# Kernel optimization log

Hardware: AMD Instinct MI355X
Metric: run time of the kernel (lower is better)

The kernel has to match this reference:

```python
import jax, jax.numpy as jnp
import numpy as np

N_USERS = 100000
EMBED_DIM = 128
N_EDGES = 640000


def setup_inputs() -> dict:
    key = jax.random.key(0)
    k1, k2, k3, k4, k5, k6 = jax.random.split(key, 6)
    # Xavier-normal-ish scale for embedding table
    emb = jax.random.normal(k1, (N_USERS, EMBED_DIM), dtype=jnp.float32) * 0.02
    s = 1.0 / np.sqrt(EMBED_DIM)
    W_l = jax.random.normal(k2, (EMBED_DIM, EMBED_DIM), dtype=jnp.float32) * s
    b_l = jax.random.normal(k3, (EMBED_DIM,), dtype=jnp.float32) * 0.01
    W_r = jax.random.normal(k4, (EMBED_DIM, EMBED_DIM), dtype=jnp.float32) * s
    src = jax.random.randint(k5, (N_EDGES,), 0, N_USERS, dtype=jnp.int64)
    dst = jax.random.randint(k6, (N_EDGES,), 0, N_USERS, dtype=jnp.int64)
    return {"emb": emb, "W_l": W_l, "b_l": b_l, "W_r": W_r, "src": src, "dst": dst}


def reference(emb, W_l, b_l, W_r, src, dst):
    # GraphSAGE (mean aggr) over the full user embedding table.
    # messages gathered from source nodes: [E, D]
    msgs = emb[src]
    agg = jax.ops.segment_sum(msgs, dst, num_segments=N_USERS)  # [N, D]
    deg = jax.ops.segment_sum(jnp.ones((dst.shape[0],), dtype=emb.dtype), dst,
                              num_segments=N_USERS)
    agg = agg / jnp.maximum(deg, 1.0)[:, None]  # mean over neighbors
    # out = lin_l(mean neighbors) + lin_r(self); bias on lin_l only (PyG SAGEConv)
    out = agg @ W_l.T + b_l + emb @ W_r.T
    # dropout (p=0) and batchnorm (is_norm=False) are identity here
    return out
```

## Files before the change

kernel.cpp:

```cpp
#include <hip/hip_runtime.h>
#include <hip/hip_bf16.h>

#define N_USERS   100000
#define EMBED_DIM 128
#define N_EDGES   640000
#define ZERO_ROW  N_USERS

typedef __bf16 bf16x8 __attribute__((ext_vector_type(8)));
typedef float  f32x4  __attribute__((ext_vector_type(4)));

#define OFF_COUNTS 25600256
#define OFF_TOTAL  26000256
#define OFF_START  26000384
#define OFF_CURSOR 26400384
#define OFF_PERM   26800384
#define OFF_WLSW   30560384
#define OFF_WRSW   30593152
#define OFF_AGGB   30625920

__device__ __forceinline__ unsigned short f2bf_rne(float f) {
    union { float f; unsigned u; } c; c.f = f;
    unsigned u = c.u + 0x7fffu + ((c.u >> 16) & 1u);
    return (unsigned short)(u >> 16);
}
__device__ __forceinline__ float bf2f_lo(unsigned u) {
    union { float f; unsigned u; } c; c.u = u << 16;
    return c.f;
}
__device__ __forceinline__ float bf2f_hi(unsigned u) {
    union { float f; unsigned u; } c; c.u = u & 0xffff0000u;
    return c.f;
}

__global__ __launch_bounds__(256) void k_init(const float* __restrict__ emb,
                                              const float* __restrict__ Wl,
                                              const float* __restrict__ Wr,
                                              const int* __restrict__ dst,
                                              unsigned short* __restrict__ embb,
                                              int* __restrict__ counts,
                                              unsigned short* __restrict__ wlsw,
                                              unsigned short* __restrict__ wrsw) {
    int i = blockIdx.x * 256 + threadIdx.x;
    if (i < 2048) {
        int li = i & 63;
        int kt = (i >> 6) & 3;
        int jt = i >> 8;
        int row  = jt * 16 + (li & 15);
        int colb = kt * 32 + ((li >> 4) << 3);
        const float4* pl = (const float4*)(Wl + row * 128 + colb);
        const float4* pr = (const float4*)(Wr + row * 128 + colb);
        float4 l0 = pl[0], l1 = pl[1];
        float4 r0 = pr[0], r1 = pr[1];
        int o = i * 8;
        wlsw[o+0] = f2bf_rne(l0.x); wlsw[o+1] = f2bf_rne(l0.y);
        wlsw[o+2] = f2bf_rne(l0.z); wlsw[o+3] = f2bf_rne(l0.w);
        wlsw[o+4] = f2bf_rne(l1.x); wlsw[o+5] = f2bf_rne(l1.y);
        wlsw[o+6] = f2bf_rne(l1.z); wlsw[o+7] = f2bf_rne(l1.w);
        wrsw[o+0] = f2bf_rne(r0.x); wrsw[o+1] = f2bf_rne(r0.y);
        wrsw[o+2] = f2bf_rne(r0.z); wrsw[o+3] = f2bf_rne(r0.w);
        wrsw[o+4] = f2bf_rne(r1.x); wrsw[o+5] = f2bf_rne(r1.y);
        wrsw[o+6] = f2bf_rne(r1.z); wrsw[o+7] = f2bf_rne(r1.w);
    }
    if (i < 16) {
        int4 z = {0, 0, 0, 0};
        ((int4*)(embb + (size_t)ZERO_ROW * EMBED_DIM))[i] = z;
    }
    float4 a = ((const float4*)emb)[i * 2 + 0];
    float4 b = ((const float4*)emb)[i * 2 + 1];
    int4 p;
    p.x = (int)f2bf_rne(a.x) | ((int)f2bf_rne(a.y) << 16);
    p.y = (int)f2bf_rne(a.z) | ((int)f2bf_rne(a.w) << 16);
    p.z = (int)f2bf_rne(b.x) | ((int)f2bf_rne(b.y) << 16);
    p.w = (int)f2bf_rne(b.z) | ((int)f2bf_rne(b.w) << 16);
    ((int4*)embb)[i] = p;
    if (i < N_EDGES) atomicAdd(&counts[dst[i]], 1);
}

__global__ __launch_bounds__(256) void k_alloc(const int* __restrict__ counts,
                                               int* __restrict__ start,
                                               int* __restrict__ cursor,
                                               int* __restrict__ total,
                                               int* __restrict__ perm) {
    int i    = blockIdx.x * 256 + threadIdx.x;
    int lane = threadIdx.x & 63;
    int wv   = threadIdx.x >> 6;
    int4 c4 = {0, 0, 0, 0};
    if (i < 25000) c4 = ((const int4*)counts)[i];
    int4 p4;
    p4.x = (c4.x + 3) & ~3;
    p4.y = (c4.y + 3) & ~3;
    p4.z = (c4.z + 3) & ~3;
    p4.w = (c4.w + 3) & ~3;
    int csum = p4.x + p4.y + p4.z + p4.w;
    int pre = csum;
#pragma unroll
    for (int d = 1; d < 64; d <<= 1) {
        int v = __shfl_up(pre, d);
        if (lane >= d) pre += v;
    }
    __shared__ int swv[4];
    __shared__ int sgbase;
    if (lane == 63) swv[wv] = pre;
    __syncthreads();
    if (threadIdx.x == 0)
        sgbase = atomicAdd(total, swv[0] + swv[1] + swv[2] + swv[3]);
    __syncthreads();
    int waveoff = 0;
    for (int w = 0; w < wv; w++) waveoff += swv[w];
    int base = sgbase + waveoff + (pre - csum);
    if (i < 25000) {
        int4 s;
        s.x = base;
        s.y = s.x + p4.x;
        s.z = s.y + p4.y;
        s.w = s.z + p4.z;
        ((int4*)start)[i]  = s;
        ((int4*)cursor)[i] = s;
        for (int k = c4.x; k < p4.x; k++) perm[s.x + k] = ZERO_ROW;
        for (int k = c4.y; k < p4.y; k++) perm[s.y + k] = ZERO_ROW;
        for (int k = c4.z; k < p4.z; k++) perm[s.z + k] = ZERO_ROW;
        for (int k = c4.w; k < p4.w; k++) perm[s.w + k] = ZERO_ROW;
    }
}

__global__ __launch_bounds__(256) void k_perm(const int* __restrict__ src,
                                              const int* __restrict__ dst,
                                              int* __restrict__ cursor,
                                              int* __restrict__ perm) {
    int e = blockIdx.x * 256 + threadIdx.x;
    if (e < N_EDGES) {
        int pos = atomicAdd(&cursor[dst[e]], 1);
        perm[pos] = src[e];
    }
}

__global__ __launch_bounds__(256) void k_aggregate(const unsigned short* __restrict__ embb,
                                                   const int* __restrict__ start,
                                                   const int* __restrict__ counts,
                                                   const int* __restrict__ perm,
                                                   unsigned short* __restrict__ aggb) {
    int gw   = (blockIdx.x * 256 + threadIdx.x) >> 6;
    int lane = threadIdx.x & 63;
    int nA = gw * 2;
    int nB = nA + 1;
    int sA = start[nA], cntA = counts[nA];
    int sB = start[nB], cntB = counts[nB];
    int ga = (cntA + 3) >> 2;
    int gb = (cntB + 3) >> 2;
    int gmin = ga < gb ? ga : gb;
    float2 accA = {0.f, 0.f}, accB = {0.f, 0.f};
    const unsigned short* ep = embb;
    int off = lane * 2;

    int t = 0;
    for (; t < gmin; t++) {
        int4 ia = ((const int4*)(perm + sA))[t];
        int4 ib = ((const int4*)(perm + sB))[t];
        unsigned a0 = *(const unsigned*)(ep + (size_t)ia.x * EMBED_DIM + off);
        unsigned a1 = *(const unsigned*)(ep + (size_t)ia.y * EMBED_DIM + off);
        unsigned a2 = *(const unsigned*)(ep + (size_t)ia.z * EMBED_DIM + off);
        unsigned a3 = *(const unsigned*)(ep + (size_t)ia.w * EMBED_DIM + off);
        unsigned b0 = *(const unsigned*)(ep + (size_t)ib.x * EMBED_DIM + off);
        unsigned b1 = *(const unsigned*)(ep + (size_t)ib.y * EMBED_DIM + off);
        unsigned b2 = *(const unsigned*)(ep + (size_t)ib.z * EMBED_DIM + off);
        unsigned b3 = *(const unsigned*)(ep + (size_t)ib.w * EMBED_DIM + off);
        accA.x += (bf2f_lo(a0) + bf2f_lo(a1)) + (bf2f_lo(a2) + bf2f_lo(a3));
        accA.y += (bf2f_hi(a0) + bf2f_hi(a1)) + (bf2f_hi(a2) + bf2f_hi(a3));
        accB.x += (bf2f_lo(b0) + bf2f_lo(b1)) + (bf2f_lo(b2) + bf2f_lo(b3));
        accB.y += (bf2f_hi(b0) + bf2f_hi(b1)) + (bf2f_hi(b2) + bf2f_hi(b3));
    }
    for (int ta = t; ta < ga; ta++) {
        int4 ia = ((const int4*)(perm + sA))[ta];
        unsigned a0 = *(const unsigned*)(ep + (size_t)ia.x * EMBED_DIM + off);
        unsigned a1 = *(const unsigned*)(ep + (size_t)ia.y * EMBED_DIM + off);
        unsigned a2 = *(const unsigned*)(ep + (size_t)ia.z * EMBED_DIM + off);
        unsigned a3 = *(const unsigned*)(ep + (size_t)ia.w * EMBED_DIM + off);
        accA.x += (bf2f_lo(a0) + bf2f_lo(a1)) + (bf2f_lo(a2) + bf2f_lo(a3));
        accA.y += (bf2f_hi(a0) + bf2f_hi(a1)) + (bf2f_hi(a2) + bf2f_hi(a3));
    }
    for (int tb = t; tb < gb; tb++) {
        int4 ib = ((const int4*)(perm + sB))[tb];
        unsigned b0 = *(const unsigned*)(ep + (size_t)ib.x * EMBED_DIM + off);
        unsigned b1 = *(const unsigned*)(ep + (size_t)ib.y * EMBED_DIM + off);
        unsigned b2 = *(const unsigned*)(ep + (size_t)ib.z * EMBED_DIM + off);
        unsigned b3 = *(const unsigned*)(ep + (size_t)ib.w * EMBED_DIM + off);
        accB.x += (bf2f_lo(b0) + bf2f_lo(b1)) + (bf2f_lo(b2) + bf2f_lo(b3));
        accB.y += (bf2f_hi(b0) + bf2f_hi(b1)) + (bf2f_hi(b2) + bf2f_hi(b3));
    }
    float invA = (cntA > 0) ? 1.0f / (float)cntA : 0.0f;
    float invB = (cntB > 0) ? 1.0f / (float)cntB : 0.0f;
    unsigned oA = (unsigned)f2bf_rne(accA.x * invA) | ((unsigned)f2bf_rne(accA.y * invA) << 16);
    unsigned oB = (unsigned)f2bf_rne(accB.x * invB) | ((unsigned)f2bf_rne(accB.y * invB) << 16);
    *(unsigned*)(aggb + (size_t)nA * EMBED_DIM + off) = oA;
    *(unsigned*)(aggb + (size_t)nB * EMBED_DIM + off) = oB;
}

#define LDS_S 136
__global__ __launch_bounds__(256) void k_matmul(const unsigned short* __restrict__ aggb,
                                                const unsigned short* __restrict__ wlsw,
                                                const unsigned short* __restrict__ wrsw,
                                                const unsigned short* __restrict__ embb,
                                                const float* __restrict__ bl,
                                                float* __restrict__ out) {
    __shared__ unsigned short sa[32 * LDS_S];
    __shared__ unsigned short se[32 * LDS_S];
    int tid  = threadIdx.x;
    int wave = tid >> 6;
    int lane = tid & 63;
    int quad = lane >> 4;
    int m    = lane & 15;
    int jt0  = wave * 2;
    int node0 = blockIdx.x * 32;

    bf16x8 wl[2][4], wr[2][4];
#pragma unroll
    for (int jj = 0; jj < 2; jj++) {
#pragma unroll
        for (int kt = 0; kt < 4; kt++) {
            size_t o = (size_t)((((jt0 + jj) * 4 + kt) * 64 + lane)) * 8;
            wl[jj][kt] = *(const bf16x8*)((const __bf16*)wlsw + o);
            wr[jj][kt] = *(const bf16x8*)((const __bf16*)wrsw + o);
        }
    }
    float bias[2];
    bias[0] = bl[(jt0 + 0) * 16 + m];
    bias[1] = bl[(jt0 + 1) * 16 + m];

    const int4* aslab = (const int4*)(aggb + (size_t)node0 * EMBED_DIM);
    const int4* eslab = (const int4*)(embb + (size_t)node0 * EMBED_DIM);
#pragma unroll
    for (int p = 0; p < 2; p++) {
        int g   = p * 256 + tid;
        int row = g >> 4;
        int c   = g & 15;
        int4 va = aslab[g];
        int4 ve = eslab[g];
        *(int4*)(sa + row * LDS_S + c * 8) = va;
        *(int4*)(se + row * LDS_S + c * 8) = ve;
    }
    __syncthreads();

    bf16x8 af[2][4], ef[2][4];
#pragma unroll
    for (int rt = 0; rt < 2; rt++) {
#pragma unroll
        for (int kt = 0; kt < 4; kt++) {
            int o = (rt * 16 + m) * LDS_S + kt * 32 + quad * 8;
            af[rt][kt] = *(const bf16x8*)(sa + o);
            ef[rt][kt] = *(const bf16x8*)(se + o);
        }
    }

#pragma unroll
    for (int rt = 0; rt < 2; rt++) {
        f32x4 acc[2] = {{0.f,0.f,0.f,0.f}, {0.f,0.f,0.f,0.f}};
#pragma unroll
        for (int kt = 0; kt < 4; kt++) {
#pragma unroll
            for (int jj = 0; jj < 2; jj++) {
                acc[jj] = __builtin_amdgcn_mfma_f32_16x16x32_bf16(af[rt][kt], wl[jj][kt], acc[jj], 0, 0, 0);
                acc[jj] = __builtin_amdgcn_mfma_f32_16x16x32_bf16(ef[rt][kt], wr[jj][kt], acc[jj], 0, 0, 0);
            }
        }
#pragma unroll
        for (int jj = 0; jj < 2; jj++) {
#pragma unroll
            for (int r = 0; r < 4; r++) {
                int orow = node0 + rt * 16 + quad * 4 + r;
                out[(size_t)orow * EMBED_DIM + (jt0 + jj) * 16 + m] = acc[jj][r] + bias[jj];
            }
        }
    }
}

extern "C" void kernel_launch(void* const* d_in, const int* in_sizes, int n_in,
                              void* d_out, int out_size, void* d_ws, size_t ws_size,
                              hipStream_t stream) {
    const float* emb = (const float*)d_in[0];
    const float* Wl  = (const float*)d_in[1];
    const float* bl  = (const float*)d_in[2];
    const float* Wr  = (const float*)d_in[3];
    const int*   src = (const int*)d_in[4];
    const int*   dst = (const int*)d_in[5];
    float* out = (float*)d_out;

    char* ws = (char*)d_ws;
    unsigned short* embb   = (unsigned short*)ws;
    int*            counts = (int*)(ws + OFF_COUNTS);
    int*            total  = (int*)(ws + OFF_TOTAL);
    int*            start  = (int*)(ws + OFF_START);
    int*            cursor = (int*)(ws + OFF_CURSOR);
    int*            perm   = (int*)(ws + OFF_PERM);
    unsigned short* wlsw   = (unsigned short*)(ws + OFF_WLSW);
    unsigned short* wrsw   = (unsigned short*)(ws + OFF_WRSW);
    unsigned short* aggb   = (unsigned short*)(ws + OFF_AGGB);

    hipMemsetAsync(ws + OFF_COUNTS, 0, (OFF_TOTAL - OFF_COUNTS) + 4, stream);

    k_init<<<6250, 256, 0, stream>>>(emb, Wl, Wr, dst, embb, counts, wlsw, wrsw);
    k_alloc<<<98, 256, 0, stream>>>(counts, start, cursor, total, perm);
    k_perm<<<2500, 256, 0, stream>>>(src, dst, cursor, perm);
    k_aggregate<<<12500, 256, 0, stream>>>(embb, start, counts, perm, aggb);
    k_matmul<<<3125, 256, 0, stream>>>(aggb, wlsw, wrsw, embb, bl, out);
}
```

Baseline: 213.1 us.

## Aggregate one node per wave with 16B row loads and cross-lane reduction

The aggregation kernel now assigns one node per wavefront instead of two. Each group of 16 lanes reads a full 256-byte bf16 row with 16-byte loads, and the four groups handle different neighbors in parallel. Partial sums are combined with xor shuffles before one group writes the result. This replaces many 4-byte gathers with wider loads and doubles the grid size, at the cost of shuffle reductions and idle lanes on low-degree nodes. It relies on perm segments for each node being padded to multiples of 4 with zero-row entries, as the previous int4 reads implied.

```diff
diff --git a/kernel.cpp b/kernel.cpp
--- a/kernel.cpp
+++ b/kernel.cpp
@@ -139,60 +139,61 @@
                                                    const int* __restrict__ counts,
                                                    const int* __restrict__ perm,
                                                    unsigned short* __restrict__ aggb) {
-    int gw   = (blockIdx.x * 256 + threadIdx.x) >> 6;
+    int node = (blockIdx.x * 256 + threadIdx.x) >> 6;
     int lane = threadIdx.x & 63;
-    int nA = gw * 2;
-    int nB = nA + 1;
-    int sA = start[nA], cntA = counts[nA];
-    int sB = start[nB], cntB = counts[nB];
-    int ga = (cntA + 3) >> 2;
-    int gb = (cntB + 3) >> 2;
-    int gmin = ga < gb ? ga : gb;
-    float2 accA = {0.f, 0.f}, accB = {0.f, 0.f};
+    int q    = lane >> 4;
+    int c    = lane & 15;
+    int s0  = start[node];
+    int cnt = counts[node];
+    int g   = (cnt + 3) >> 2;
+
+    float acc[8] = {0.f,0.f,0.f,0.f,0.f,0.f,0.f,0.f};
     const unsigned short* ep = embb;
-    int off = lane * 2;
+    int co = c * 8;
 
     int t = 0;
-    for (; t < gmin; t++) {
-        int4 ia = ((const int4*)(perm + sA))[t];
-        int4 ib = ((const int4*)(perm + sB))[t];
-        unsigned a0 = *(const unsigned*)(ep + (size_t)ia.x * EMBED_DIM + off);
-        unsigned a1 = *(const unsigned*)(ep + (size_t)ia.y * EMBED_DIM + off);
-        unsigned a2 = *(const unsigned*)(ep + (size_t)ia.z * EMBED_DIM + off);
-        unsigned a3 = *(const unsigned*)(ep + (size_t)ia.w * EMBED_DIM + off);
-        unsigned b0 = *(const unsigned*)(ep + (size_t)ib.x * EMBED_DIM + off);
-        unsigned b1 = *(const unsigned*)(ep + (size_t)ib.y * EMBED_DIM + off);
-        unsigned b2 = *(const unsigned*)(ep + (size_t)ib.z * EMBED_DIM + off);
-        unsigned b3 = *(const unsigned*)(ep + (size_t)ib.w * EMBED_DIM + off);
-        accA.x += (bf2f_lo(a0) + bf2f_lo(a1)) + (bf2f_lo(a2) + bf2f_lo(a3));
-        accA.y += (bf2f_hi(a0) + bf2f_hi(a1)) + (bf2f_hi(a2) + bf2f_hi(a3));
-        accB.x += (bf2f_lo(b0) + bf2f_lo(b1)) + (bf2f_lo(b2) + bf2f_lo(b3));
-        accB.y += (bf2f_hi(b0) + bf2f_hi(b1)) + (bf2f_hi(b2) + bf2f_hi(b3));
-    }
-    for (int ta = t; ta < ga; ta++) {
-        int4 ia = ((const int4*)(perm + sA))[ta];
-        unsigned a0 = *(const unsigned*)(ep + (size_t)ia.x * EMBED_DIM + off);
-        unsigned a1 = *(const unsigned*)(ep + (size_t)ia.y * EMBED_DIM + off);
-        unsigned a2 = *(const unsigned*)(ep + (size_t)ia.z * EMBED_DIM + off);
-        unsigned a3 = *(const unsigned*)(ep + (size_t)ia.w * EMBED_DIM + off);
-        accA.x += (bf2f_lo(a0) + bf2f_lo(a1)) + (bf2f_lo(a2) + bf2f_lo(a3));
-        accA.y += (bf2f_hi(a0) + bf2f_hi(a1)) + (bf2f_hi(a2) + bf2f_hi(a3));
-    }
-    for (int tb = t; tb < gb; tb++) {
-        int4 ib = ((const int4*)(perm + sB))[tb];
-        unsigned b0 = *(const unsigned*)(ep + (size_t)ib.x * EMBED_DIM + off);
-        unsigned b1 = *(const unsigned*)(ep + (size_t)ib.y * EMBED_DIM + off);
-        unsigned b2 = *(const unsigned*)(ep + (size_t)ib.z * EMBED_DIM + off);
-        unsigned b3 = *(const unsigned*)(ep + (size_t)ib.w * EMBED_DIM + off);
-        accB.x += (bf2f_lo(b0) + bf2f_lo(b1)) + (bf2f_lo(b2) + bf2f_lo(b3));
-        accB.y += (bf2f_hi(b0) + bf2f_hi(b1)) + (bf2f_hi(b2) + bf2f_hi(b3));
-    }
-    float invA = (cntA > 0) ? 1.0f / (float)cntA : 0.0f;
-    float invB = (cntB > 0) ? 1.0f / (float)cntB : 0.0f;
-    unsigned oA = (unsigned)f2bf_rne(accA.x * invA) | ((unsigned)f2bf_rne(accA.y * invA) << 16);
-    unsigned oB = (unsigned)f2bf_rne(accB.x * invB) | ((unsigned)f2bf_rne(accB.y * invB) << 16);
-    *(unsigned*)(aggb + (size_t)nA * EMBED_DIM + off) = oA;
-    *(unsigned*)(aggb + (size_t)nB * EMBED_DIM + off) = oB;
+    for (; t + 1 < g; t += 2) {
+        int r0 = perm[s0 + t * 4 + q];
+        int r1 = perm[s0 + t * 4 + 4 + q];
+        uint4 v0 = *(const uint4*)(ep + (size_t)r0 * EMBED_DIM + co);
+        uint4 v1 = *(const uint4*)(ep + (size_t)r1 * EMBED_DIM + co);
+        acc[0] += bf2f_lo(v0.x) + bf2f_lo(v1.x);
+        acc[1] += bf2f_hi(v0.x) + bf2f_hi(v1.x);
+        acc[2] += bf2f_lo(v0.y) + bf2f_lo(v1.y);
+        acc[3] += bf2f_hi(v0.y) + bf2f_hi(v1.y);
+        acc[4] += bf2f_lo(v0.z) + bf2f_lo(v1.z);
+        acc[5] += bf2f_hi(v0.z) + bf2f_hi(v1.z);
+        acc[6] += bf2f_lo(v0.w) + bf2f_lo(v1.w);
+        acc[7] += bf2f_hi(v0.w) + bf2f_hi(v1.w);
+    }
+    if (t < g) {
+        int r0 = perm[s0 + t * 4 + q];
+        uint4 v0 = *(const uint4*)(ep + (size_t)r0 * EMBED_DIM + co);
+        acc[0] += bf2f_lo(v0.x);
+        acc[1] += bf2f_hi(v0.x);
+        acc[2] += bf2f_lo(v0.y);
+        acc[3] += bf2f_hi(v0.y);
+        acc[4] += bf2f_lo(v0.z);
+        acc[5] += bf2f_hi(v0.z);
+        acc[6] += bf2f_lo(v0.w);
+        acc[7] += bf2f_hi(v0.w);
+    }
+
+#pragma unroll
+    for (int i = 0; i < 8; i++) {
+        acc[i] += __shfl_xor(acc[i], 16, 64);
+        acc[i] += __shfl_xor(acc[i], 32, 64);
+    }
+
+    if (q == 0) {
+        float inv = (cnt > 0) ? 1.0f / (float)cnt : 0.0f;
+        uint4 o;
+        o.x = (unsigned)f2bf_rne(acc[0] * inv) | ((unsigned)f2bf_rne(acc[1] * inv) << 16);
+        o.y = (unsigned)f2bf_rne(acc[2] * inv) | ((unsigned)f2bf_rne(acc[3] * inv) << 16);
+        o.z = (unsigned)f2bf_rne(acc[4] * inv) | ((unsigned)f2bf_rne(acc[5] * inv) << 16);
+        o.w = (unsigned)f2bf_rne(acc[6] * inv) | ((unsigned)f2bf_rne(acc[7] * inv) << 16);
+        *(uint4*)(aggb + (size_t)node * EMBED_DIM + co) = o;
+    }
 }
 
 #define LDS_S 136
@@ -232,11 +233,11 @@
     for (int p = 0; p < 2; p++) {
         int g   = p * 256 + tid;
         int row = g >> 4;
-        int c   = g & 15;
+        int cc  = g & 15;
         int4 va = aslab[g];
         int4 ve = eslab[g];
-        *(int4*)(sa + row * LDS_S + c * 8) = va;
-        *(int4*)(se + row * LDS_S + c * 8) = ve;
+        *(int4*)(sa + row * LDS_S + cc * 8) = va;
+        *(int4*)(se + row * LDS_S + cc * 8) = ve;
     }
     __syncthreads();
 
@@ -300,6 +301,6 @@
     k_init<<<6250, 256, 0, stream>>>(emb, Wl, Wr, dst, embb, counts, wlsw, wrsw);
     k_alloc<<<98, 256, 0, stream>>>(counts, start, cursor, total, perm);
     k_perm<<<2500, 256, 0, stream>>>(src, dst, cursor, perm);
-    k_aggregate<<<12500, 256, 0, stream>>>(embb, start, counts, perm, aggb);
+    k_aggregate<<<25000, 256, 0, stream>>>(embb, start, counts, perm, aggb);
     k_matmul<<<3125, 256, 0, stream>>>(aggb, wlsw, wrsw, embb, bl, out);
 }
```

Measured after the change: 218.3 us. +2.4%, slower.
